# Optimization experiments

Hardware: AMD Instinct MI355X
Metric: run time of the kernel (lower is better)

The kernel has to match this reference:

```python
import jax, jax.numpy as jnp
import numpy as np

MARGIN = 0.1
LAMBDA_EFFECT = 0.5

B, T_V, K, T_S = 32, 8192, 64, 128


def setup_inputs() -> dict:
    key = jax.random.key(0)
    k1, k2, k3, k4, k5 = jax.random.split(key, 5)
    pred_orig = jax.random.normal(k1, (B, T_V), dtype=jnp.float32)
    pred_intervened = jax.random.normal(k2, (K, B, T_V), dtype=jnp.float32)
    intervened_indices = jax.random.randint(k3, (K,), 0, T_S, dtype=jnp.int32)
    # GT alignment mask: sparse-ish binary alignment between frames and sentences
    gt_mask = jax.random.bernoulli(k4, 0.2, (B, T_V, T_S)).astype(jnp.int32)
    # prefix-valid video mask: valid length per batch in [T_V//2, T_V]
    lengths = jax.random.randint(k5, (B,), T_V // 2, T_V + 1, dtype=jnp.int32)
    mask_video = (jnp.arange(T_V, dtype=jnp.int32)[None, :] < lengths[:, None]).astype(jnp.int32)
    return {
        "pred_orig": pred_orig,
        "pred_intervened": pred_intervened,
        "intervened_indices": intervened_indices,
        "gt_mask": gt_mask,
        "mask_video": mask_video,
    }


def reference(pred_orig, pred_intervened, intervened_indices, gt_mask, mask_video):
    # pred_orig: [B,T], pred_intervened: [K,B,T], gt_mask: [B,T,S], mask_video: [B,T]
    prob_orig = jax.nn.sigmoid(pred_orig)                 # [B,T]
    prob_int = jax.nn.sigmoid(pred_intervened)            # [K,B,T]
    effect = jnp.abs(prob_orig[None, :, :] - prob_int)    # [K,B,T]

    valid = mask_video.astype(bool)                       # [B,T] (prefix mask == :T_v_valid slice)
    # gather intervened sentence columns: [B,T,K] -> [K,B,T]
    gt_sel = jnp.transpose(gt_mask[:, :, intervened_indices], (2, 0, 1))

    aligned = (gt_sel > 0) & valid[None]                  # [K,B,T]
    non_aligned = (gt_sel == 0) & valid[None]             # [K,B,T]

    cnt_a = aligned.sum(axis=-1)                          # [K,B]
    cnt_n = non_aligned.sum(axis=-1)                      # [K,B]

    ea = jnp.sum(effect * aligned, axis=-1) / jnp.maximum(cnt_a, 1)
    en = jnp.sum(effect * non_aligned, axis=-1) / jnp.maximum(cnt_n, 1)

    per_pair = jnp.where((cnt_a > 0) & (cnt_n > 0),
                         jax.nn.relu(MARGIN - (ea - en)),
                         jnp.zeros_like(ea))
    num_interventions = pred_orig.shape[0] * pred_intervened.shape[0]
    alignment_consistency = per_pair.sum() / max(num_interventions, 1)
    total_intervention_loss = alignment_consistency * LAMBDA_EFFECT
    return alignment_consistency, total_intervention_loss
```

## Files before the change

### kernel.cpp

```cpp
#include <hip/hip_runtime.h>
#include <cstdint>

#define BB 32
#define TV 8192
#define KK 64
#define TS 128
#define MARGIN_F 0.1f
#define LAMBDA_F 0.5f

typedef unsigned long long u64;
typedef unsigned int u32;

static constexpr int KB_PAIRS = KK * BB;
static constexpr int W32_PER_B = TV / 32;
static constexpr int W64_PER_B = TV / 64;


__global__ __launch_bounds__(256) void plane_kernel(
    const int* __restrict__ idx, const int* __restrict__ gt,
    const int* __restrict__ mv, u32* __restrict__ vbit, u32* __restrict__ pl,
    int* __restrict__ len, int* __restrict__ mw) {
  const int lane = threadIdx.x & 63;
  const int w = threadIdx.x >> 6;
  const int blk = blockIdx.x;
  const int b = blk >> 6;
  const int tile = blk & 63;
  const int g2 = tile * 4 + w;
  const int grow = b * TV + g2 * 32;

  const int mvv = (lane < 32) ? mv[grow + lane] : 0;
  const u32 V32 = (u32)__ballot(mvv != 0);
  if (lane == 0) {
    vbit[b * W32_PER_B + g2] = V32;
    if (V32) {
      atomicAdd(&len[b], __popc(V32));
      atomicMax(&mw[b], g2);
    }
  }

  u32 plane = 0;
  if (V32) {
    const int c = idx[lane];
    const int* col = gt + (size_t)grow * TS + c;
    int v[32];
#pragma unroll
    for (int r = 0; r < 32; ++r) v[r] = col[r * TS];
#pragma unroll
    for (int r = 0; r < 32; ++r)
      if (v[r] > 0) plane |= 1u << r;
    plane &= V32;
  }
  pl[(size_t)(b * KK + lane) * W32_PER_B + g2] = plane;
}

__global__ __launch_bounds__(256, 4) void reduce_kernel(
    const float* __restrict__ po, const float* __restrict__ pi,
    const u32* __restrict__ vbit, const u32* __restrict__ pl,
    const int* __restrict__ mw,
    float* __restrict__ gsa, float* __restrict__ gsv,
    float* __restrict__ gca) {
  const int tid = threadIdx.x;
  const int lane = tid & 63;
  const int w = tid >> 6;
  const int kb = blockIdx.x;
  const int b = kb & (BB - 1);
  const int k = kb >> 5;
  const u64* plrow = (const u64*)pl + (size_t)(b * KK + k) * W64_PER_B;
  const u64* vrow = (const u64*)vbit + (size_t)b * W64_PER_B;
  const float* pirow = pi + (size_t)kb * TV;
  const float* porow = po + (size_t)b * TV;

  __shared__ float rs[4][2];
  __shared__ int rca;
  if (tid == 0) rca = 0;
  __syncthreads();

  const int nch = min(8, (mw[b] + 32) >> 5);
  const int sh = (tid & 15) * 4;
  float sa = 0.f, sv = 0.f;
#pragma unroll 2
  for (int c = 0; c < nch; ++c) {
    const int t = c * 1024 + tid * 4;
    const int widx = t >> 6;
    const u64 vw = vrow[widx];
    const u32 vb4 = (u32)((vw >> sh) & 15ull);
    if (vb4) {
      const u64 aw = plrow[widx];
      const u32 ab4 = (u32)((aw >> sh) & 15ull);
      const float4 x = *(const float4*)(pirow + t);
      const float4 p = *(const float4*)(porow + t);
      const float e0 =
          fabsf(__fdividef(1.f, 1.f + __expf(-p.x)) -
                __fdividef(1.f, 1.f + __expf(-x.x)));
      const float e1 =
          fabsf(__fdividef(1.f, 1.f + __expf(-p.y)) -
                __fdividef(1.f, 1.f + __expf(-x.y)));
      const float e2 =
          fabsf(__fdividef(1.f, 1.f + __expf(-p.z)) -
                __fdividef(1.f, 1.f + __expf(-x.z)));
      const float e3 =
          fabsf(__fdividef(1.f, 1.f + __expf(-p.w)) -
                __fdividef(1.f, 1.f + __expf(-x.w)));
      if (vb4 & 1u) sv += e0;
      if (vb4 & 2u) sv += e1;
      if (vb4 & 4u) sv += e2;
      if (vb4 & 8u) sv += e3;
      if (ab4 & 1u) sa += e0;
      if (ab4 & 2u) sa += e1;
      if (ab4 & 4u) sa += e2;
      if (ab4 & 8u) sa += e3;
    }
  }
#pragma unroll
  for (int off = 32; off; off >>= 1) {
    sa += __shfl_xor(sa, off);
    sv += __shfl_xor(sv, off);
  }
  if (lane == 0) {
    rs[w][0] = sa;
    rs[w][1] = sv;
  }
  if (tid < W64_PER_B) atomicAdd(&rca, __popcll(plrow[tid]));
  __syncthreads();
  if (tid == 0) {
    gsa[kb] = rs[0][0] + rs[1][0] + rs[2][0] + rs[3][0];
    gsv[kb] = rs[0][1] + rs[1][1] + rs[2][1] + rs[3][1];
    gca[kb] = (float)rca;
  }
}

__global__ __launch_bounds__(256) void fin_kernel(
    const float* __restrict__ gsa, const float* __restrict__ gsv,
    const float* __restrict__ gca, const int* __restrict__ len,
    float* __restrict__ out) {
  float s = 0.f;
  for (int i = threadIdx.x; i < KB_PAIRS; i += 256) {
    const int b = i & (BB - 1);
    const float ca = gca[i];
    const float cn = (float)len[b] - ca;
    if (ca > 0.f && cn > 0.f) {
      const float sa = gsa[i];
      const float sv = gsv[i];
      const float d = MARGIN_F - (sa / ca - (sv - sa) / cn);
      s += d > 0.f ? d : 0.f;
    }
  }
#pragma unroll
  for (int off = 32; off > 0; off >>= 1) s += __shfl_down(s, off);
  __shared__ float ws4[4];
  if ((threadIdx.x & 63) == 0) ws4[threadIdx.x >> 6] = s;
  __syncthreads();
  if (threadIdx.x == 0) {
    const float S = ws4[0] + ws4[1] + ws4[2] + ws4[3];
    const float ac = S * (1.0f / (float)KB_PAIRS);
    out[0] = ac;
    out[1] = ac * LAMBDA_F;
  }
}

extern "C" void kernel_launch(void* const* d_in, const int* in_sizes, int n_in,
                              void* d_out, int out_size, void* d_ws, size_t ws_size,
                              hipStream_t stream) {
  const float* pred_orig = (const float*)d_in[0];
  const float* pred_int  = (const float*)d_in[1];
  const int*   idx       = (const int*)d_in[2];
  const int*   gt        = (const int*)d_in[3];
  const int*   mv        = (const int*)d_in[4];
  float* out = (float*)d_out;

  float* gsa = (float*)d_ws;
  float* gsv = gsa + KB_PAIRS;
  float* gca = gsv + KB_PAIRS;
  int*   len = (int*)(gca + KB_PAIRS);
  int*   mw  = len + BB;
  u32*   vbit = (u32*)(mw + BB);
  u32*   pl   = vbit + BB * W32_PER_B;

  hipMemsetAsync(len, 0, 2 * BB * sizeof(int), stream);
  plane_kernel<<<BB * 64, 256, 0, stream>>>(idx, gt, mv, vbit, pl, len, mw);
  reduce_kernel<<<KB_PAIRS, 256, 0, stream>>>(pred_orig, pred_int, vbit, pl,
                                              mw, gsa, gsv, gca);
  fin_kernel<<<1, 256, 0, stream>>>(gsa, gsv, gca, len, out);
}
```

Before: 306.6 us.

## Build bitplanes for all sentences via contiguous LDS tile loads, gather columns in reduce

The plane kernel no longer does strided per-lane column gathers of the 64 selected sentences. Each 64-thread block copies a contiguous 32-row by 128-column tile of the alignment mask into LDS with global_load_lds, then builds bitmasks for all 128 sentences in an interleaved layout. The reduce kernel now applies the intervened-index gather itself, reading the selected sentence's 64-bit word with a TS stride and masking it with validity. This swaps latency-bound scattered reads for coalesced ones, at the cost of computing twice as many planes and more strided plane reads in the reduce step.

```diff
diff --git a/kernel.cpp b/kernel.cpp
--- a/kernel.cpp
+++ b/kernel.cpp
@@ -16,17 +16,17 @@
 static constexpr int W64_PER_B = TV / 64;
 
 
-__global__ __launch_bounds__(256) void plane_kernel(
-    const int* __restrict__ idx, const int* __restrict__ gt,
-    const int* __restrict__ mv, u32* __restrict__ vbit, u32* __restrict__ pl,
+__global__ __launch_bounds__(64) void plane_kernel(
+    const int* __restrict__ gt, const int* __restrict__ mv,
+    u32* __restrict__ vbit, u32* __restrict__ pl,
     int* __restrict__ len, int* __restrict__ mw) {
-  const int lane = threadIdx.x & 63;
-  const int w = threadIdx.x >> 6;
+  const int lane = threadIdx.x;
   const int blk = blockIdx.x;
-  const int b = blk >> 6;
-  const int tile = blk & 63;
-  const int g2 = tile * 4 + w;
+  const int b = blk >> 8;
+  const int g2 = blk & 255;
   const int grow = b * TV + g2 * 32;
+
+  __shared__ __align__(16) int gtile[32 * TS];
 
   const int mvv = (lane < 32) ? mv[grow + lane] : 0;
   const u32 V32 = (u32)__ballot(mvv != 0);
@@ -38,23 +38,42 @@
     }
   }
 
-  u32 plane = 0;
-  if (V32) {
-    const int c = idx[lane];
-    const int* col = gt + (size_t)grow * TS + c;
-    int v[32];
-#pragma unroll
-    for (int r = 0; r < 32; ++r) v[r] = col[r * TS];
+  const int g64 = g2 >> 1, h = g2 & 1;
+  u32* outp = pl + ((size_t)(b * 128 + g64) * TS) * 2 + h;
+
+  if (V32 == 0u) {
+    outp[2 * lane] = 0u;
+    outp[2 * (lane + 64)] = 0u;
+    return;
+  }
+
+  {
+    const char* gsrc = (const char*)(gt + (size_t)grow * TS);
+    char* ldst = (char*)gtile;
+#pragma unroll
+    for (int i = 0; i < 16; ++i) {
+      __builtin_amdgcn_global_load_lds(
+          (const __attribute__((address_space(1))) u32*)(gsrc + i * 1024 +
+                                                         lane * 16),
+          (__attribute__((address_space(3))) u32*)(ldst + i * 1024), 16, 0, 0);
+    }
+  }
+  __syncthreads();
+
+#pragma unroll
+  for (int p = 0; p < 2; ++p) {
+    const int s = lane + 64 * p;
+    u32 wbits = 0;
 #pragma unroll
     for (int r = 0; r < 32; ++r)
-      if (v[r] > 0) plane |= 1u << r;
-    plane &= V32;
-  }
-  pl[(size_t)(b * KK + lane) * W32_PER_B + g2] = plane;
+      if (gtile[r * TS + s] > 0) wbits |= 1u << r;
+    outp[2 * s] = wbits & V32;
+  }
 }
 
 __global__ __launch_bounds__(256, 4) void reduce_kernel(
     const float* __restrict__ po, const float* __restrict__ pi,
+    const int* __restrict__ idx,
     const u32* __restrict__ vbit, const u32* __restrict__ pl,
     const int* __restrict__ mw,
     float* __restrict__ gsa, float* __restrict__ gsv,
@@ -65,7 +84,8 @@
   const int kb = blockIdx.x;
   const int b = kb & (BB - 1);
   const int k = kb >> 5;
-  const u64* plrow = (const u64*)pl + (size_t)(b * KK + k) * W64_PER_B;
+  const int c = idx[k];
+  const u64* plb = (const u64*)pl + (size_t)b * (128 * TS) + c;
   const u64* vrow = (const u64*)vbit + (size_t)b * W64_PER_B;
   const float* pirow = pi + (size_t)kb * TV;
   const float* porow = po + (size_t)b * TV;
@@ -79,13 +99,13 @@
   const int sh = (tid & 15) * 4;
   float sa = 0.f, sv = 0.f;
 #pragma unroll 2
-  for (int c = 0; c < nch; ++c) {
-    const int t = c * 1024 + tid * 4;
+  for (int cc = 0; cc < nch; ++cc) {
+    const int t = cc * 1024 + tid * 4;
     const int widx = t >> 6;
     const u64 vw = vrow[widx];
     const u32 vb4 = (u32)((vw >> sh) & 15ull);
     if (vb4) {
-      const u64 aw = plrow[widx];
+      const u64 aw = plb[(size_t)widx * TS] & vw;
       const u32 ab4 = (u32)((aw >> sh) & 15ull);
       const float4 x = *(const float4*)(pirow + t);
       const float4 p = *(const float4*)(porow + t);
@@ -120,7 +140,8 @@
     rs[w][0] = sa;
     rs[w][1] = sv;
   }
-  if (tid < W64_PER_B) atomicAdd(&rca, __popcll(plrow[tid]));
+  if (tid < W64_PER_B)
+    atomicAdd(&rca, __popcll(plb[(size_t)tid * TS] & vrow[tid]));
   __syncthreads();
   if (tid == 0) {
     gsa[kb] = rs[0][0] + rs[1][0] + rs[2][0] + rs[3][0];
@@ -177,8 +198,8 @@
   u32*   pl   = vbit + BB * W32_PER_B;
 
   hipMemsetAsync(len, 0, 2 * BB * sizeof(int), stream);
-  plane_kernel<<<BB * 64, 256, 0, stream>>>(idx, gt, mv, vbit, pl, len, mw);
-  reduce_kernel<<<KB_PAIRS, 256, 0, stream>>>(pred_orig, pred_int, vbit, pl,
-                                              mw, gsa, gsv, gca);
+  plane_kernel<<<BB * W32_PER_B, 64, 0, stream>>>(gt, mv, vbit, pl, len, mw);
+  reduce_kernel<<<KB_PAIRS, 256, 0, stream>>>(pred_orig, pred_int, idx, vbit,
+                                              pl, mw, gsa, gsv, gca);
   fin_kernel<<<1, 256, 0, stream>>>(gsa, gsv, gca, len, out);
 }
```

Result: faster. 282.4 us (-7.9%).
